# Performance work log

Measured on AMD Instinct MI355X. Metric: run time of the kernel, lower is better.

Reference implementation:

```python
import jax, jax.numpy as jnp
import numpy as np

EPS = 1e-6   # param.eps
DT = 1e-2    # param.dt
DX = 1.0     # param.dx
DY = 1.0     # param.dy
N_PARAM = 1.0  # param.N


def _lap(c, dx=1.0, dy=1.0):
    # 5-point periodic Laplacian stencil on the last two dims
    return ((jnp.roll(c, 1, -1) + jnp.roll(c, -1, -1) - 2.0 * c) / (dx * dx)
            + (jnp.roll(c, 1, -2) + jnp.roll(c, -1, -2) - 2.0 * c) / (dy * dy))


def _log_with_mask(m, eps=EPS):
    # masked positions get constant eps -> zero gradient there, like torch masked_fill
    return jnp.log(jnp.where(m < eps, eps, m))


def setup_inputs() -> dict:
    key = jax.random.key(0)
    ks = jax.random.split(key, 12)
    B, H, W = 8, 1024, 1024
    inp = {
        "cv": jax.random.uniform(ks[0], (B, H, W), dtype=jnp.float32),
        "ci": jax.random.uniform(ks[1], (B, H, W), dtype=jnp.float32),
        "eta": jax.random.uniform(ks[2], (B, H, W), dtype=jnp.float32),
    }
    names = ["energy_v0", "energy_i0", "kBT0", "kappa_v0", "kappa_i0",
             "kappa_eta0", "diff_v0", "diff_i0", "L0"]
    for i, n in enumerate(names):
        inp[n] = jax.random.uniform(ks[3 + i], (1,), dtype=jnp.float32)
    return inp


def reference(cv, ci, eta, energy_v0, energy_i0, kBT0, kappa_v0, kappa_i0,
              kappa_eta0, diff_v0, diff_i0, L0):
    energy_v = jnp.abs(energy_v0) + 0.001
    energy_i = jnp.abs(energy_i0) + 0.001
    kBT = jnp.abs(kBT0) + 0.001
    kappa_v = jnp.abs(kappa_v0) + 0.001
    kappa_i = jnp.abs(kappa_i0) + 0.001
    kappa_eta = jnp.abs(kappa_eta0) + 0.001
    diff_v = jnp.abs(diff_v0) + 0.001
    diff_i = jnp.abs(diff_i0) + 0.001
    L = jnp.abs(L0) + 0.001

    lap_cv = _lap(cv, DX, DY)
    lap_ci = _lap(ci, DX, DY)
    lap_eta = _lap(eta, DX, DY)

    h = (eta - 1.0) ** 2
    j = eta ** 2
    cs = 1.0 - cv - ci
    log_cv = _log_with_mask(cv)
    log_ci = _log_with_mask(ci)
    log_cs = _log_with_mask(cs)

    fs = energy_v * cv + energy_i * ci + kBT * (cv * log_cv + ci * log_ci + cs * log_cs)
    dfs_dcv = energy_v + kBT * (log_cv - log_cs)
    dfs_dci = energy_i + kBT * (log_ci - log_cs)

    fv = (cv - 1.0) ** 2 + ci ** 2
    dfv_dcv = 2.0 * (cv - 1.0)
    dfv_dci = 2.0 * ci

    dF_dcv = h * dfs_dcv + j * dfv_dcv - kappa_v * lap_cv
    dF_dci = h * dfs_dci + j * dfv_dci - kappa_i * lap_ci
    dF_deta = N_PARAM * (fs * 2.0 * (eta - 1.0) + fv * 2.0 * eta - kappa_eta * lap_eta)

    mv = diff_v * cv / kBT
    mi = diff_i * ci / kBT

    cv_new = jnp.clip(cv + DT * (mv * _lap(dF_dcv)), 0.0, 1.0)
    ci_new = jnp.clip(ci + DT * (mi * _lap(dF_dci)), 0.0, 1.0)
    eta_new = jnp.clip(eta + DT * (-L * dF_deta), 0.0, 1.0)
    return cv_new, ci_new, eta_new
```

## Files before the change

### kernel.cpp

```cpp
#include <hip/hip_runtime.h>

#define WMASK 1023
#define LOG2W 10
#define HW (1024 * 1024)

#define EPS 1e-6f
#define DT 1e-2f

#define TX 64
#define TY 16

#define RCH 18
#define RST 72

#define DCH 18
#define DYT 18

typedef float f4 __attribute__((ext_vector_type(4)));

__device__ __forceinline__ float scal(const float* __restrict__ p) {
    return fabsf(p[0]) + 0.001f;
}
__device__ __forceinline__ float clip01(float v) {
    return fminf(fmaxf(v, 0.0f), 1.0f);
}
__device__ __forceinline__ float lg2m(float m) {
    return __log2f(fmaxf(m, EPS));
}

__global__ __launch_bounds__(256) void irr_fused(
    const float* __restrict__ cv,
    const float* __restrict__ ci,
    const float* __restrict__ eta,
    const float* __restrict__ p_ev,
    const float* __restrict__ p_ei,
    const float* __restrict__ p_kbt,
    const float* __restrict__ p_kv,
    const float* __restrict__ p_ki,
    const float* __restrict__ p_ke,
    const float* __restrict__ p_dv,
    const float* __restrict__ p_di,
    const float* __restrict__ p_L,
    float* __restrict__ cv_new,
    float* __restrict__ ci_new,
    float* __restrict__ eta_new)
{
    __shared__ float scv[20][RST];
    __shared__ float sci[20][RST];
    __shared__ float seta[18][RST];
    __shared__ float sdv[DYT][RST];
    __shared__ float sdi[DYT][RST];

    const int tid = threadIdx.x;
    const int x0 = blockIdx.x * TX;
    const int y0 = blockIdx.y * TY;
    const int bbase = blockIdx.z * HW;

    const float energy_v = scal(p_ev);
    const float energy_i = scal(p_ei);
    const float kBT      = scal(p_kbt);
    const float kappa_v  = scal(p_kv);
    const float kappa_i  = scal(p_ki);
    const float kappa_e  = scal(p_ke);
    const float diff_v   = scal(p_dv);
    const float diff_i   = scal(p_di);
    const float L        = scal(p_L);
    const float rv = diff_v / kBT;
    const float ri = diff_i / kBT;
    const float kl = kBT * 0.69314718056f;

    for (int t = tid; t < 1044; t += 256) {
        const float* __restrict__ src;
        float (*dstA)[RST];
        int r, gy0;
        if (t < 360)      { src = cv;  r = t;       gy0 = y0 - 2; dstA = scv; }
        else if (t < 720) { src = ci;  r = t - 360; gy0 = y0 - 2; dstA = sci; }
        else              { src = eta; r = t - 720; gy0 = y0 - 1; dstA = seta; }
        const int cx = r % RCH;
        const int cy = r / RCH;
        const int gx = (x0 - 4 + (cx << 2)) & WMASK;
        const int gy = (gy0 + cy) & WMASK;
        const f4 v = *(const f4*)(src + bbase + (gy << LOG2W) + gx);
        *(f4*)&dstA[cy][cx << 2] = v;
    }
    __syncthreads();

    for (int t = tid; t < DCH * DYT; t += 256) {
        const int k  = t % DCH;
        const int ey = t / DCH;
        const int rx = k << 2;
        const int ry = ey + 1;

        const f4 cC = *(const f4*)&scv[ry][rx];
        const f4 cU = *(const f4*)&scv[ry - 1][rx];
        const f4 cD = *(const f4*)&scv[ry + 1][rx];
        const f4 iC = *(const f4*)&sci[ry][rx];
        const f4 iU = *(const f4*)&sci[ry - 1][rx];
        const f4 iD = *(const f4*)&sci[ry + 1][rx];
        const f4 eC = *(const f4*)&seta[ey][rx];
        const int eyU = (ey == 0)  ? 0  : ey - 1;
        const int eyD = (ey == 17) ? 17 : ey + 1;
        const f4 eU = *(const f4*)&seta[eyU][rx];
        const f4 eD = *(const f4*)&seta[eyD][rx];

        float cL, cR, iL, iR, eL, eR;
        if (k == 0) {
            const int gofs = bbase + (((y0 - 1 + ey) & WMASK) << LOG2W) + ((x0 - 5) & WMASK);
            cL = cv[gofs]; iL = ci[gofs]; eL = 0.0f;
        } else {
            cL = scv[ry][rx - 1]; iL = sci[ry][rx - 1]; eL = seta[ey][rx - 1];
        }
        if (k == DCH - 1) {
            const int gofs = bbase + (((y0 - 1 + ey) & WMASK) << LOG2W) + ((x0 + 68) & WMASK);
            cR = cv[gofs]; iR = ci[gofs]; eR = 0.0f;
        } else {
            cR = scv[ry][rx + 4]; iR = sci[ry][rx + 4]; eR = seta[ey][rx + 4];
        }

        f4 dv, di, en;
        #pragma unroll
        for (int j = 0; j < 4; ++j) {
            const float c0 = cC[j];
            const float i0 = iC[j];
            const float e0 = eC[j];
            const float cl = (j == 0) ? cL : cC[j - 1];
            const float cr = (j == 3) ? cR : cC[j + 1];
            const float il = (j == 0) ? iL : iC[j - 1];
            const float ir = (j == 3) ? iR : iC[j + 1];
            const float el = (j == 0) ? eL : eC[j - 1];
            const float er = (j == 3) ? eR : eC[j + 1];

            const float lap_cv  = cl + cr + cU[j] + cD[j] - 4.0f * c0;
            const float lap_ci  = il + ir + iU[j] + iD[j] - 4.0f * i0;
            const float lap_eta = el + er + eU[j] + eD[j] - 4.0f * e0;

            const float h  = (e0 - 1.0f) * (e0 - 1.0f);
            const float jj = e0 * e0;
            const float cs = 1.0f - c0 - i0;
            const float lgv = lg2m(c0);
            const float lgi = lg2m(i0);
            const float lgs = lg2m(cs);

            const float dfs_dcv = energy_v + kl * (lgv - lgs);
            const float dfs_dci = energy_i + kl * (lgi - lgs);

            dv[j] = h * dfs_dcv + jj * (2.0f * (c0 - 1.0f)) - kappa_v * lap_cv;
            di[j] = h * dfs_dci + jj * (2.0f * i0)          - kappa_i * lap_ci;

            const float fs = energy_v * c0 + energy_i * i0
                           + kl * (c0 * lgv + i0 * lgi + cs * lgs);
            const float fv = (c0 - 1.0f) * (c0 - 1.0f) + i0 * i0;
            const float dF_deta = fs * 2.0f * (e0 - 1.0f) + fv * 2.0f * e0
                                - kappa_e * lap_eta;
            en[j] = clip01(e0 + DT * (-L * dF_deta));
        }

        *(f4*)&sdv[ey][rx] = dv;
        *(f4*)&sdi[ey][rx] = di;

        if (k >= 1 && k <= 16 && ey >= 1 && ey <= 16) {
            const int gidx = bbase + ((y0 - 1 + ey) << LOG2W)
                           + (x0 - 4 + (k << 2));
            __builtin_nontemporal_store(en, (f4*)(eta_new + gidx));
        }
    }
    __syncthreads();

    {
        const int ox4 = tid & 15;
        const int oy  = tid >> 4;
        const int ex  = (ox4 << 2) + 4;
        const int ey  = oy + 1;

        const f4    vC = *(const f4*)&sdv[ey][ex];
        const float vL = sdv[ey][ex - 1];
        const float vR = sdv[ey][ex + 4];
        const f4    vU = *(const f4*)&sdv[ey - 1][ex];
        const f4    vD = *(const f4*)&sdv[ey + 1][ex];

        const f4    wC = *(const f4*)&sdi[ey][ex];
        const float wL = sdi[ey][ex - 1];
        const float wR = sdi[ey][ex + 4];
        const f4    wU = *(const f4*)&sdi[ey - 1][ex];
        const f4    wD = *(const f4*)&sdi[ey + 1][ex];

        const f4 c0 = *(const f4*)&scv[oy + 2][ex];
        const f4 i0 = *(const f4*)&sci[oy + 2][ex];

        const int gidx = bbase + ((y0 + oy) << LOG2W) + (x0 + (ox4 << 2));

        f4 outv, outi;
        #pragma unroll
        for (int j = 0; j < 4; ++j) {
            const float lv = ((j == 0) ? vL : vC[j - 1])
                           + ((j == 3) ? vR : vC[j + 1])
                           + vU[j] + vD[j] - 4.0f * vC[j];
            const float li = ((j == 0) ? wL : wC[j - 1])
                           + ((j == 3) ? wR : wC[j + 1])
                           + wU[j] + wD[j] - 4.0f * wC[j];
            outv[j] = clip01(c0[j] + DT * ((rv * c0[j]) * lv));
            outi[j] = clip01(i0[j] + DT * ((ri * i0[j]) * li));
        }
        __builtin_nontemporal_store(outv, (f4*)(cv_new + gidx));
        __builtin_nontemporal_store(outi, (f4*)(ci_new + gidx));
    }
}

extern "C" void kernel_launch(void* const* d_in, const int* in_sizes, int n_in,
                              void* d_out, int out_size, void* d_ws, size_t ws_size,
                              hipStream_t stream) {
    const float* cv  = (const float*)d_in[0];
    const float* ci  = (const float*)d_in[1];
    const float* eta = (const float*)d_in[2];
    const float* p_ev  = (const float*)d_in[3];
    const float* p_ei  = (const float*)d_in[4];
    const float* p_kbt = (const float*)d_in[5];
    const float* p_kv  = (const float*)d_in[6];
    const float* p_ki  = (const float*)d_in[7];
    const float* p_ke  = (const float*)d_in[8];
    const float* p_dv  = (const float*)d_in[9];
    const float* p_di  = (const float*)d_in[10];
    const float* p_L   = (const float*)d_in[11];

    const int N = in_sizes[0];

    float* out     = (float*)d_out;
    float* cv_new  = out;
    float* ci_new  = out + N;
    float* eta_new = out + 2 * N;

    const dim3 block(256);
    const dim3 grid(1024 / TX, 1024 / TY, N / HW);

    irr_fused<<<grid, block, 0, stream>>>(cv, ci, eta, p_ev, p_ei, p_kbt,
                                          p_kv, p_ki, p_ke, p_dv, p_di, p_L,
                                          cv_new, ci_new, eta_new);
}
```

Measured before the change: 212.6 us.

## Compute only interior dF per thread and evaluate tile halo on demand

Measured after the change: 212.4 us. No clear change (-0.1%).

```diff
diff --git a/kernel.cpp b/kernel.cpp
--- a/kernel.cpp
+++ b/kernel.cpp
@@ -12,9 +12,7 @@
 
 #define RCH 18
 #define RST 72
-
-#define DCH 18
-#define DYT 18
+#define SST 64
 
 typedef float f4 __attribute__((ext_vector_type(4)));
 
@@ -28,7 +26,7 @@
     return __log2f(fmaxf(m, EPS));
 }
 
-__global__ __launch_bounds__(256) void irr_fused(
+__global__ __launch_bounds__(256, 6) void irr_fused(
     const float* __restrict__ cv,
     const float* __restrict__ ci,
     const float* __restrict__ eta,
@@ -45,11 +43,11 @@
     float* __restrict__ ci_new,
     float* __restrict__ eta_new)
 {
-    __shared__ float scv[20][RST];
-    __shared__ float sci[20][RST];
-    __shared__ float seta[18][RST];
-    __shared__ float sdv[DYT][RST];
-    __shared__ float sdi[DYT][RST];
+    __shared__ __attribute__((aligned(16))) float scv[20][RST];
+    __shared__ __attribute__((aligned(16))) float sci[20][RST];
+    __shared__ __attribute__((aligned(16))) float seta[18][RST];
+    __shared__ __attribute__((aligned(16))) float sdv[16][SST];
+    __shared__ __attribute__((aligned(16))) float sdi[16][SST];
 
     const int tid = threadIdx.x;
     const int x0 = blockIdx.x * TX;
@@ -65,9 +63,10 @@
     const float diff_v   = scal(p_dv);
     const float diff_i   = scal(p_di);
     const float L        = scal(p_L);
-    const float rv = diff_v / kBT;
-    const float ri = diff_i / kBT;
-    const float kl = kBT * 0.69314718056f;
+    const float kl   = kBT * 0.69314718056f;
+    const float dtl  = DT * L;
+    const float dtrv = DT * diff_v / kBT;
+    const float dtri = DT * diff_i / kBT;
 
     for (int t = tid; t < 1044; t += 256) {
         const float* __restrict__ src;
@@ -85,125 +84,143 @@
     }
     __syncthreads();
 
-    for (int t = tid; t < DCH * DYT; t += 256) {
-        const int k  = t % DCH;
-        const int ey = t / DCH;
-        const int rx = k << 2;
-        const int ry = ey + 1;
-
-        const f4 cC = *(const f4*)&scv[ry][rx];
-        const f4 cU = *(const f4*)&scv[ry - 1][rx];
-        const f4 cD = *(const f4*)&scv[ry + 1][rx];
-        const f4 iC = *(const f4*)&sci[ry][rx];
-        const f4 iU = *(const f4*)&sci[ry - 1][rx];
-        const f4 iD = *(const f4*)&sci[ry + 1][rx];
-        const f4 eC = *(const f4*)&seta[ey][rx];
-        const int eyU = (ey == 0)  ? 0  : ey - 1;
-        const int eyD = (ey == 17) ? 17 : ey + 1;
-        const f4 eU = *(const f4*)&seta[eyU][rx];
-        const f4 eD = *(const f4*)&seta[eyD][rx];
-
-        float cL, cR, iL, iR, eL, eR;
-        if (k == 0) {
-            const int gofs = bbase + (((y0 - 1 + ey) & WMASK) << LOG2W) + ((x0 - 5) & WMASK);
-            cL = cv[gofs]; iL = ci[gofs]; eL = 0.0f;
-        } else {
-            cL = scv[ry][rx - 1]; iL = sci[ry][rx - 1]; eL = seta[ey][rx - 1];
-        }
-        if (k == DCH - 1) {
-            const int gofs = bbase + (((y0 - 1 + ey) & WMASK) << LOG2W) + ((x0 + 68) & WMASK);
-            cR = cv[gofs]; iR = ci[gofs]; eR = 0.0f;
-        } else {
-            cR = scv[ry][rx + 4]; iR = sci[ry][rx + 4]; eR = seta[ey][rx + 4];
-        }
-
-        f4 dv, di, en;
+    const int k  = tid & 15;
+    const int ey = tid >> 4;
+    const int rx = (k << 2) + 4;
+
+    const f4    cC = *(const f4*)&scv[ey + 2][rx];
+    const f4    cU = *(const f4*)&scv[ey + 1][rx];
+    const f4    cD = *(const f4*)&scv[ey + 3][rx];
+    const float cL = scv[ey + 2][rx - 1];
+    const float cR = scv[ey + 2][rx + 4];
+
+    const f4    iC = *(const f4*)&sci[ey + 2][rx];
+    const f4    iU = *(const f4*)&sci[ey + 1][rx];
+    const f4    iD = *(const f4*)&sci[ey + 3][rx];
+    const float iL = sci[ey + 2][rx - 1];
+    const float iR = sci[ey + 2][rx + 4];
+
+    const f4    eC = *(const f4*)&seta[ey + 1][rx];
+    const f4    eU = *(const f4*)&seta[ey][rx];
+    const f4    eD = *(const f4*)&seta[ey + 2][rx];
+    const float eL = seta[ey + 1][rx - 1];
+    const float eR = seta[ey + 1][rx + 4];
+
+    f4 dv, di, en;
+    #pragma unroll
+    for (int j = 0; j < 4; ++j) {
+        const float c0 = cC[j];
+        const float i0 = iC[j];
+        const float e0 = eC[j];
+        const float cl = (j == 0) ? cL : cC[j - 1];
+        const float cr = (j == 3) ? cR : cC[j + 1];
+        const float il = (j == 0) ? iL : iC[j - 1];
+        const float ir = (j == 3) ? iR : iC[j + 1];
+        const float el = (j == 0) ? eL : eC[j - 1];
+        const float er = (j == 3) ? eR : eC[j + 1];
+
+        const float lap_cv  = cl + cr + cU[j] + cD[j] - 4.0f * c0;
+        const float lap_ci  = il + ir + iU[j] + iD[j] - 4.0f * i0;
+        const float lap_eta = el + er + eU[j] + eD[j] - 4.0f * e0;
+
+        const float h  = (e0 - 1.0f) * (e0 - 1.0f);
+        const float jj = e0 * e0;
+        const float cs = 1.0f - c0 - i0;
+        const float lgv = lg2m(c0);
+        const float lgi = lg2m(i0);
+        const float lgs = lg2m(cs);
+
+        dv[j] = h * (energy_v + kl * (lgv - lgs)) + jj * (2.0f * (c0 - 1.0f))
+              - kappa_v * lap_cv;
+        di[j] = h * (energy_i + kl * (lgi - lgs)) + jj * (2.0f * i0)
+              - kappa_i * lap_ci;
+
+        const float fs = energy_v * c0 + energy_i * i0
+                       + kl * (c0 * lgv + i0 * lgi + cs * lgs);
+        const float fv = (c0 - 1.0f) * (c0 - 1.0f) + i0 * i0;
+        const float dF_deta = fs * 2.0f * (e0 - 1.0f) + fv * 2.0f * e0
+                            - kappa_e * lap_eta;
+        en[j] = clip01(fmaf(-dtl, dF_deta, e0));
+    }
+
+    const int c = k << 2;
+    *(f4*)&sdv[ey][c] = dv;
+    *(f4*)&sdi[ey][c] = di;
+
+    const int gidx = bbase + ((y0 + ey) << LOG2W) + (x0 + c);
+    __builtin_nontemporal_store(en, (f4*)(eta_new + gidx));
+
+    __syncthreads();
+
+    auto evalpt = [&](int cr, int cc, int er) -> float2 {
+        const float c0 = scv[cr][cc];
+        const float lap_cv = scv[cr][cc - 1] + scv[cr][cc + 1]
+                           + scv[cr - 1][cc] + scv[cr + 1][cc] - 4.0f * c0;
+        const float i0 = sci[cr][cc];
+        const float lap_ci = sci[cr][cc - 1] + sci[cr][cc + 1]
+                           + sci[cr - 1][cc] + sci[cr + 1][cc] - 4.0f * i0;
+        const float e0 = seta[er][cc];
+        const float h  = (e0 - 1.0f) * (e0 - 1.0f);
+        const float jj = e0 * e0;
+        const float cs = 1.0f - c0 - i0;
+        const float lgv = lg2m(c0);
+        const float lgi = lg2m(i0);
+        const float lgs = lg2m(cs);
+        const float dvx = h * (energy_v + kl * (lgv - lgs))
+                        + jj * (2.0f * (c0 - 1.0f)) - kappa_v * lap_cv;
+        const float dix = h * (energy_i + kl * (lgi - lgs))
+                        + jj * (2.0f * i0) - kappa_i * lap_ci;
+        return make_float2(dvx, dix);
+    };
+
+    float vL, wL, vR, wR;
+    if (k == 0) {
+        const float2 r = evalpt(ey + 2, 3, ey + 1);
+        vL = r.x; wL = r.y;
+    } else {
+        vL = sdv[ey][c - 1]; wL = sdi[ey][c - 1];
+    }
+    if (k == 15) {
+        const float2 r = evalpt(ey + 2, 68, ey + 1);
+        vR = r.x; wR = r.y;
+    } else {
+        vR = sdv[ey][c + 4]; wR = sdi[ey][c + 4];
+    }
+
+    f4 vU, wU, vD, wD;
+    if (ey == 0) {
         #pragma unroll
         for (int j = 0; j < 4; ++j) {
-            const float c0 = cC[j];
-            const float i0 = iC[j];
-            const float e0 = eC[j];
-            const float cl = (j == 0) ? cL : cC[j - 1];
-            const float cr = (j == 3) ? cR : cC[j + 1];
-            const float il = (j == 0) ? iL : iC[j - 1];
-            const float ir = (j == 3) ? iR : iC[j + 1];
-            const float el = (j == 0) ? eL : eC[j - 1];
-            const float er = (j == 3) ? eR : eC[j + 1];
-
-            const float lap_cv  = cl + cr + cU[j] + cD[j] - 4.0f * c0;
-            const float lap_ci  = il + ir + iU[j] + iD[j] - 4.0f * i0;
-            const float lap_eta = el + er + eU[j] + eD[j] - 4.0f * e0;
-
-            const float h  = (e0 - 1.0f) * (e0 - 1.0f);
-            const float jj = e0 * e0;
-            const float cs = 1.0f - c0 - i0;
-            const float lgv = lg2m(c0);
-            const float lgi = lg2m(i0);
-            const float lgs = lg2m(cs);
-
-            const float dfs_dcv = energy_v + kl * (lgv - lgs);
-            const float dfs_dci = energy_i + kl * (lgi - lgs);
-
-            dv[j] = h * dfs_dcv + jj * (2.0f * (c0 - 1.0f)) - kappa_v * lap_cv;
-            di[j] = h * dfs_dci + jj * (2.0f * i0)          - kappa_i * lap_ci;
-
-            const float fs = energy_v * c0 + energy_i * i0
-                           + kl * (c0 * lgv + i0 * lgi + cs * lgs);
-            const float fv = (c0 - 1.0f) * (c0 - 1.0f) + i0 * i0;
-            const float dF_deta = fs * 2.0f * (e0 - 1.0f) + fv * 2.0f * e0
-                                - kappa_e * lap_eta;
-            en[j] = clip01(e0 + DT * (-L * dF_deta));
+            const float2 r = evalpt(1, rx + j, 0);
+            vU[j] = r.x; wU[j] = r.y;
         }
-
-        *(f4*)&sdv[ey][rx] = dv;
-        *(f4*)&sdi[ey][rx] = di;
-
-        if (k >= 1 && k <= 16 && ey >= 1 && ey <= 16) {
-            const int gidx = bbase + ((y0 - 1 + ey) << LOG2W)
-                           + (x0 - 4 + (k << 2));
-            __builtin_nontemporal_store(en, (f4*)(eta_new + gidx));
-        }
-    }
-    __syncthreads();
-
-    {
-        const int ox4 = tid & 15;
-        const int oy  = tid >> 4;
-        const int ex  = (ox4 << 2) + 4;
-        const int ey  = oy + 1;
-
-        const f4    vC = *(const f4*)&sdv[ey][ex];
-        const float vL = sdv[ey][ex - 1];
-        const float vR = sdv[ey][ex + 4];
-        const f4    vU = *(const f4*)&sdv[ey - 1][ex];
-        const f4    vD = *(const f4*)&sdv[ey + 1][ex];
-
-        const f4    wC = *(const f4*)&sdi[ey][ex];
-        const float wL = sdi[ey][ex - 1];
-        const float wR = sdi[ey][ex + 4];
-        const f4    wU = *(const f4*)&sdi[ey - 1][ex];
-        const f4    wD = *(const f4*)&sdi[ey + 1][ex];
-
-        const f4 c0 = *(const f4*)&scv[oy + 2][ex];
-        const f4 i0 = *(const f4*)&sci[oy + 2][ex];
-
-        const int gidx = bbase + ((y0 + oy) << LOG2W) + (x0 + (ox4 << 2));
-
-        f4 outv, outi;
+    } else {
+        vU = *(const f4*)&sdv[ey - 1][c];
+        wU = *(const f4*)&sdi[ey - 1][c];
+    }
+    if (ey == 15) {
         #pragma unroll
         for (int j = 0; j < 4; ++j) {
-            const float lv = ((j == 0) ? vL : vC[j - 1])
-                           + ((j == 3) ? vR : vC[j + 1])
-                           + vU[j] + vD[j] - 4.0f * vC[j];
-            const float li = ((j == 0) ? wL : wC[j - 1])
-                           + ((j == 3) ? wR : wC[j + 1])
-                           + wU[j] + wD[j] - 4.0f * wC[j];
-            outv[j] = clip01(c0[j] + DT * ((rv * c0[j]) * lv));
-            outi[j] = clip01(i0[j] + DT * ((ri * i0[j]) * li));
+            const float2 r = evalpt(18, rx + j, 17);
+            vD[j] = r.x; wD[j] = r.y;
         }
-        __builtin_nontemporal_store(outv, (f4*)(cv_new + gidx));
-        __builtin_nontemporal_store(outi, (f4*)(ci_new + gidx));
-    }
+    } else {
+        vD = *(const f4*)&sdv[ey + 1][c];
+        wD = *(const f4*)&sdi[ey + 1][c];
+    }
+
+    f4 outv, outi;
+    #pragma unroll
+    for (int j = 0; j < 4; ++j) {
+        const float lv = ((j == 0) ? vL : dv[j - 1]) + ((j == 3) ? vR : dv[j + 1])
+                       + vU[j] + vD[j] - 4.0f * dv[j];
+        const float li = ((j == 0) ? wL : di[j - 1]) + ((j == 3) ? wR : di[j + 1])
+                       + wU[j] + wD[j] - 4.0f * di[j];
+        outv[j] = clip01(fmaf(dtrv * cC[j], lv, cC[j]));
+        outi[j] = clip01(fmaf(dtri * iC[j], li, iC[j]));
+    }
+    __builtin_nontemporal_store(outv, (f4*)(cv_new + gidx));
+    __builtin_nontemporal_store(outi, (f4*)(ci_new + gidx));
 }
 
 extern "C" void kernel_launch(void* const* d_in, const int* in_sizes, int n_in,
```
